# Kernel tuning notes

Hardware: AMD Instinct MI355X
Metric: run time of the kernel (lower is better)

## Reference

```python
import jax, jax.numpy as jnp
import numpy as np

INPUT_SIZE = 512   # num_embeddings == RNN input feature dim
SEQ = INPUT_SIZE // 4   # 128, embedding dim == RNN seq_len
HID = 12
OUT = 3
B = 2048


def setup_inputs() -> dict:
    key = jax.random.key(0)
    ks = jax.random.split(key, 12)
    s = 0.1
    x = jax.random.randint(ks[0], (B, INPUT_SIZE), 0, INPUT_SIZE)
    emb = jax.random.normal(ks[1], (INPUT_SIZE, SEQ), dtype=jnp.float32) * s
    w_ih_f = jax.random.normal(ks[2], (HID, INPUT_SIZE), dtype=jnp.float32) * s
    w_hh_f = jax.random.normal(ks[3], (HID, HID), dtype=jnp.float32) * s
    b_ih_f = jax.random.normal(ks[4], (HID,), dtype=jnp.float32) * s
    b_hh_f = jax.random.normal(ks[5], (HID,), dtype=jnp.float32) * s
    w_ih_r = jax.random.normal(ks[6], (HID, INPUT_SIZE), dtype=jnp.float32) * s
    w_hh_r = jax.random.normal(ks[7], (HID, HID), dtype=jnp.float32) * s
    b_ih_r = jax.random.normal(ks[8], (HID,), dtype=jnp.float32) * s
    b_hh_r = jax.random.normal(ks[9], (HID,), dtype=jnp.float32) * s
    fc_w = jax.random.normal(ks[10], (OUT, 2 * HID), dtype=jnp.float32) * s
    fc_b = jax.random.normal(ks[11], (OUT,), dtype=jnp.float32) * s
    return {"x": x, "emb": emb,
            "w_ih_f": w_ih_f, "w_hh_f": w_hh_f, "b_ih_f": b_ih_f, "b_hh_f": b_hh_f,
            "w_ih_r": w_ih_r, "w_hh_r": w_hh_r, "b_ih_r": b_ih_r, "b_hh_r": b_hh_r,
            "fc_w": fc_w, "fc_b": fc_b}


def reference(x, emb, w_ih_f, w_hh_f, b_ih_f, b_hh_f,
              w_ih_r, w_hh_r, b_ih_r, b_hh_r, fc_w, fc_b):
    # embedding lookup: (B, INPUT_SIZE) -> (B, INPUT_SIZE, SEQ)
    e = emb[x]
    # view(-1, input_size, seq) is a no-op on this contiguous shape; swapaxes(1,2)
    xs = jnp.swapaxes(e, 1, 2)  # (B, SEQ, INPUT_SIZE): seq_len=SEQ, feat=INPUT_SIZE

    # forward-direction tanh RNN: precompute input projections, scan the recurrence
    pre = jnp.einsum('bsi,hi->sbh', xs, w_ih_f) + b_ih_f  # (SEQ, B, HID)

    def step(h, p):
        h = jnp.tanh(p + h @ w_hh_f.T + b_hh_f)
        return h, None

    h0 = jnp.zeros((xs.shape[0], HID), dtype=xs.dtype)
    h_fwd, _ = jax.lax.scan(step, h0, pre)  # final forward hidden (B, HID)

    # reverse-direction output at the LAST timestep = one step from zero hidden
    # on x_{T-1} (only out[:, -1, :] is consumed by the module)
    h_bwd = jnp.tanh(xs[:, -1, :] @ w_ih_r.T + b_ih_r + b_hh_r)  # (B, HID)

    out_last = jnp.concatenate([h_fwd, h_bwd], axis=-1)  # (B, 2*HID)
    return out_last @ fc_w.T + fc_b  # (B, OUT)
```

## Files before the change

kernel.cpp:

```cpp
#include <hip/hip_runtime.h>
#include <hip/hip_bf16.h>

#define B_N     2048
#define IN_N    512
#define SEQ_N   128
#define HID_N   12
#define HP_N    16
#define OUT_N   3

typedef __attribute__((ext_vector_type(8))) short short8;
typedef __attribute__((ext_vector_type(4))) float f32x4;
typedef unsigned int uint;
typedef unsigned short ushort;

__device__ __forceinline__ float fast_tanh(float x) {
    float e = __builtin_amdgcn_exp2f(x * 2.8853900817779268f);
    return 1.0f - 2.0f * __builtin_amdgcn_rcpf(e + 1.0f);
}

__device__ __forceinline__ ushort f2bf(float f) {
    uint u = __float_as_uint(f);
    u += 0x7fffu + ((u >> 16) & 1u);
    return (ushort)(u >> 16);
}

__device__ __forceinline__ float bf2f(ushort s) {
    return __uint_as_float(((uint)s) << 16);
}

__global__ __launch_bounds__(256) void k_prep(
    const float* __restrict__ emb, const float* __restrict__ w_ih_f,
    const float* __restrict__ w_ih_r,
    ushort* __restrict__ embB, ushort* __restrict__ wP)
{
    int tid = blockIdx.x * 256 + threadIdx.x;
    float4 e = ((const float4*)emb)[tid];
    uint2 o;
    o.x = (uint)f2bf(e.x) | ((uint)f2bf(e.y) << 16);
    o.y = (uint)f2bf(e.z) | ((uint)f2bf(e.w) << 16);
    ((uint2*)embB)[tid] = o;

    int j   = tid & 7;
    int l   = (tid >> 3) & 63;
    int src = (tid >> 9) & 1;
    int cks = tid >> 10;
    int h   = l & 15;
    int i   = (cks >> 2) * 128 + (cks & 3) * 32 + (l >> 4) * 8 + j;
    const float* wsrc = src ? w_ih_r : w_ih_f;
    wP[(((size_t)cks * 2 + src) * 64 + l) * 8 + j] =
        (h < HID_N) ? f2bf(wsrc[h * IN_N + i]) : (ushort)0;
}

__global__ __launch_bounds__(256, 4) void k_pre(
    const int* __restrict__ x, const ushort* __restrict__ embB,
    const ushort* __restrict__ wP,
    const float* __restrict__ b_ih_r, const float* __restrict__ b_hh_r,
    ushort* __restrict__ preB, float* __restrict__ rev)
{
    __shared__ int xb[IN_N];
    __shared__ __align__(16) ushort As[128 * 128];

    const int t = threadIdx.x;
    const int b = blockIdx.x;

    ((int2*)xb)[t] = ((const int2*)(x + b * IN_N))[t];
    __syncthreads();

    const int l      = t & 63;
    const int w      = t >> 6;
    const int lane16 = l & 15;
    const int quad   = l >> 4;
    const int il     = w * 32 + quad * 8;
    const int wg     = w * 4 + quad;
    const int l7     = lane16 & 7;

    f32x4 acc[2] = {{0.f,0.f,0.f,0.f},{0.f,0.f,0.f,0.f}};
    f32x4 accR   = {0.f,0.f,0.f,0.f};

    uint R[8][4];

    #pragma unroll
    for (int j = 0; j < 8; ++j) {
        const uint4 v = *(const uint4*)(embB + (size_t)xb[il + j] * SEQ_N + lane16 * 8);
        R[j][0] = v.x; R[j][1] = v.y; R[j][2] = v.z; R[j][3] = v.w;
    }

    for (int c = 0; c < 4; ++c) {
        short8 bfr[4], bfrR[4];
        #pragma unroll
        for (int ks = 0; ks < 4; ++ks) {
            const ushort* wp = wP + ((size_t)(c * 4 + ks) * 128 + l) * 8;
            bfr[ks]  = *(const short8*)(wp);
            bfrR[ks] = *(const short8*)(wp + 512);
        }

        if (c) __syncthreads();

        #pragma unroll
        for (int p = 0; p < 8; ++p) {
            const uint sel = (p & 1) ? 0x07060302u : 0x05040100u;
            const int pv = p >> 1;
            uint u0 = __builtin_amdgcn_perm(R[1][pv], R[0][pv], sel);
            uint u1 = __builtin_amdgcn_perm(R[3][pv], R[2][pv], sel);
            uint u2 = __builtin_amdgcn_perm(R[5][pv], R[4][pv], sel);
            uint u3 = __builtin_amdgcn_perm(R[7][pv], R[6][pv], sel);
            const int s    = lane16 * 8 + p;
            const int slot = wg ^ p ^ l7;
            *(uint4*)&As[(size_t)s * 128 + (size_t)slot * 8] =
                make_uint4(u0, u1, u2, u3);
        }

        if (c < 3) {
            const int ibase = (c + 1) * 128 + il;
            #pragma unroll
            for (int j = 0; j < 8; ++j) {
                const uint4 v = *(const uint4*)(embB + (size_t)xb[ibase + j] * SEQ_N + lane16 * 8);
                R[j][0] = v.x; R[j][1] = v.y; R[j][2] = v.z; R[j][3] = v.w;
            }
        }
        __syncthreads();

        #pragma unroll
        for (int tt = 0; tt < 2; ++tt) {
            const int row = (w * 2 + tt) * 16 + lane16;
            const int fr  = (row & 7) ^ ((row >> 3) & 7);
            #pragma unroll
            for (int ks = 0; ks < 4; ++ks) {
                const int slot = (ks * 4 + quad) ^ fr;
                short8 af = *(const short8*)&As[(size_t)row * 128 + (size_t)slot * 8];
                acc[tt] = __builtin_amdgcn_mfma_f32_16x16x32_bf16(af, bfr[ks], acc[tt], 0, 0, 0);
                if (tt == 1)
                    accR = __builtin_amdgcn_mfma_f32_16x16x32_bf16(af, bfrR[ks], accR, 0, 0, 0);
            }
        }
    }

    if (lane16 < HID_N) {
        #pragma unroll
        for (int tt = 0; tt < 2; ++tt) {
            #pragma unroll
            for (int r = 0; r < 4; ++r) {
                int s = (w * 2 + tt) * 16 + quad * 4 + r;
                preB[((size_t)b * SEQ_N + s) * HP_N + lane16] = f2bf(acc[tt][r]);
            }
        }
        if (w == 3 && quad == 3)
            rev[b * HP_N + lane16] =
                fast_tanh(accR[3] + b_ih_r[lane16] + b_hh_r[lane16]);
    }
}

__global__ __launch_bounds__(256) void k_rnn(
    const ushort* __restrict__ preB, const float* __restrict__ rev,
    const float* __restrict__ w_hh_f,
    const float* __restrict__ b_ih_f, const float* __restrict__ b_hh_f,
    const float* __restrict__ fc_w, const float* __restrict__ fc_b,
    float* __restrict__ out)
{
    __shared__ float ho[16][40];

    const int tid = threadIdx.x;
    const int l   = tid & 63;
    const int j   = l & 15;
    const int jj  = (j < 12) ? j : 0;
    const int gid = tid >> 4;
    const int b   = blockIdx.x * 16 + gid;
    const int baseaddr = (l & 48) << 2;

    const float4* wr = (const float4*)(w_hh_f + jj * 12);
    float4 w0 = wr[0], w1 = wr[1], w2 = wr[2];
    float W[12] = {w0.x, w0.y, w0.z, w0.w, w1.x, w1.y, w1.z, w1.w,
                   w2.x, w2.y, w2.z, w2.w};
    const float bias = b_ih_f[jj] + b_hh_f[jj];

    const ushort* pb = preB + (size_t)b * SEQ_N * HP_N + j;
    ushort pq[8];
    #pragma unroll
    for (int k = 0; k < 8; ++k) pq[k] = pb[k * HP_N];

    float h = 0.f;
    for (int s8 = 0; s8 < 16; ++s8) {
        #pragma unroll
        for (int k = 0; k < 8; ++k) {
            int s = s8 * 8 + k;
            float p = bf2f(pq[k]) + bias;
            pq[k] = pb[((s + 8) & 127) * HP_N];
            int hb = __float_as_int(h);
            float hk[12];
            #pragma unroll
            for (int kk = 0; kk < 12; ++kk)
                hk[kk] = __int_as_float(__builtin_amdgcn_ds_bpermute(baseaddr + 4 * kk, hb));
            float c0 = p, c1 = 0.f, c2 = 0.f;
            #pragma unroll
            for (int u = 0; u < 4; ++u) {
                c0 = __builtin_fmaf(W[u],     hk[u],     c0);
                c1 = __builtin_fmaf(W[4 + u], hk[4 + u], c1);
                c2 = __builtin_fmaf(W[8 + u], hk[8 + u], c2);
            }
            h = fast_tanh(c0 + c1 + c2);
        }
    }

    ho[gid][j]      = h;
    ho[gid][20 + j] = rev[b * HP_N + j];
    if (j < OUT_N) {
        const float* fw = fc_w + j * 24;
        float o = fc_b[j];
        #pragma unroll
        for (int k = 0; k < 12; ++k)
            o += fw[k] * ho[gid][k] + fw[12 + k] * ho[gid][20 + k];
        out[b * OUT_N + j] = o;
    }
}

extern "C" void kernel_launch(void* const* d_in, const int* in_sizes, int n_in,
                              void* d_out, int out_size, void* d_ws, size_t ws_size,
                              hipStream_t stream) {
    const int*   x      = (const int*)  d_in[0];
    const float* emb    = (const float*)d_in[1];
    const float* w_ih_f = (const float*)d_in[2];
    const float* w_hh_f = (const float*)d_in[3];
    const float* b_ih_f = (const float*)d_in[4];
    const float* b_hh_f = (const float*)d_in[5];
    const float* w_ih_r = (const float*)d_in[6];
    const float* b_ih_r = (const float*)d_in[8];
    const float* b_hh_r = (const float*)d_in[9];
    const float* fc_w   = (const float*)d_in[10];
    const float* fc_b   = (const float*)d_in[11];
    float* out = (float*)d_out;

    ushort* preB = (ushort*)d_ws;
    float*  rev  = (float*)((char*)d_ws + 8388608);
    ushort* embB = (ushort*)((char*)d_ws + 8519680);
    ushort* wP   = (ushort*)((char*)d_ws + 8650752);

    k_prep<<<64,   256, 0, stream>>>(emb, w_ih_f, w_ih_r, embB, wP);
    k_pre <<<B_N,  256, 0, stream>>>(x, embB, wP, b_ih_r, b_hh_r, preB, rev);
    k_rnn <<<B_N/16,256,0, stream>>>(preB, rev, w_hh_f, b_ih_f, b_hh_f, fc_w, fc_b, out);
}
```

Measured before the change: 127.1 us.

## Process four batches per k_pre block with LDS-staged weights and software-pipelined gathers

k_pre now handles four batch rows per block, staging the packed bf16 input-projection weights once into LDS and reusing them across all 16 chunk iterations. Gather indices are prefetched two chunks ahead straight from global memory, replacing the shared index buffer, and embedding row loads overlap the MFMA work of the previous chunk, with explicit barriers around the As tile. This amortizes weight loads and block launch overhead. In exchange LDS use doubles, occupancy is capped at 2 blocks per CU, and the grid shrinks to 512 blocks.

```diff
diff --git a/kernel.cpp b/kernel.cpp
--- a/kernel.cpp
+++ b/kernel.cpp
@@ -51,21 +51,16 @@
         (h < HID_N) ? f2bf(wsrc[h * IN_N + i]) : (ushort)0;
 }
 
-__global__ __launch_bounds__(256, 4) void k_pre(
+__global__ __launch_bounds__(256, 2) void k_pre(
     const int* __restrict__ x, const ushort* __restrict__ embB,
     const ushort* __restrict__ wP,
     const float* __restrict__ b_ih_r, const float* __restrict__ b_hh_r,
     ushort* __restrict__ preB, float* __restrict__ rev)
 {
-    __shared__ int xb[IN_N];
     __shared__ __align__(16) ushort As[128 * 128];
-
-    const int t = threadIdx.x;
-    const int b = blockIdx.x;
-
-    ((int2*)xb)[t] = ((const int2*)(x + b * IN_N))[t];
-    __syncthreads();
-
+    __shared__ __align__(16) ushort wPs[16384];
+
+    const int t      = threadIdx.x;
     const int l      = t & 63;
     const int w      = t >> 6;
     const int lane16 = l & 15;
@@ -73,52 +68,78 @@
     const int il     = w * 32 + quad * 8;
     const int wg     = w * 4 + quad;
     const int l7     = lane16 & 7;
-
-    f32x4 acc[2] = {{0.f,0.f,0.f,0.f},{0.f,0.f,0.f,0.f}};
-    f32x4 accR   = {0.f,0.f,0.f,0.f};
-
+    const int so     = lane16 * 8;
+    const int b0     = blockIdx.x * 4;
+
+    {
+        const uint4* s4 = (const uint4*)wP;
+        uint4*       d4 = (uint4*)wPs;
+        #pragma unroll
+        for (int i = 0; i < 8; ++i) d4[t + i * 256] = s4[t + i * 256];
+    }
+
+    f32x4 acc0 = {0.f,0.f,0.f,0.f};
+    f32x4 acc1 = {0.f,0.f,0.f,0.f};
+    f32x4 accR = {0.f,0.f,0.f,0.f};
     uint R[8][4];
 
-    #pragma unroll
-    for (int j = 0; j < 8; ++j) {
-        const uint4 v = *(const uint4*)(embB + (size_t)xb[il + j] * SEQ_N + lane16 * 8);
-        R[j][0] = v.x; R[j][1] = v.y; R[j][2] = v.z; R[j][3] = v.w;
-    }
-
-    for (int c = 0; c < 4; ++c) {
-        short8 bfr[4], bfrR[4];
-        #pragma unroll
-        for (int ks = 0; ks < 4; ++ks) {
-            const ushort* wp = wP + ((size_t)(c * 4 + ks) * 128 + l) * 8;
-            bfr[ks]  = *(const short8*)(wp);
-            bfrR[ks] = *(const short8*)(wp + 512);
-        }
-
-        if (c) __syncthreads();
-
-        #pragma unroll
-        for (int p = 0; p < 8; ++p) {
-            const uint sel = (p & 1) ? 0x07060302u : 0x05040100u;
-            const int pv = p >> 1;
+#define LD8(k, ix) { uint4 v = *(const uint4*)(embB + (size_t)(ix) * SEQ_N + so); \
+        R[k][0]=v.x; R[k][1]=v.y; R[k][2]=v.z; R[k][3]=v.w; }
+
+    int4 nA, nB;
+    {
+        const int* xq = x + (size_t)b0 * IN_N + il;
+        nA = *(const int4*)xq;
+        nB = *(const int4*)(xq + 4);
+    }
+    LD8(0, nA.x) LD8(1, nA.y) LD8(2, nA.z) LD8(3, nA.w)
+    LD8(4, nB.x) LD8(5, nB.y) LD8(6, nB.z) LD8(7, nB.w)
+    {
+        const int* xq = x + (size_t)b0 * IN_N + 128 + il;
+        nA = *(const int4*)xq;
+        nB = *(const int4*)(xq + 4);
+    }
+
+    for (int p = 0; p < 16; ++p) {
+        const int c = p & 3;
+
+        #pragma unroll
+        for (int pp = 0; pp < 8; ++pp) {
+            const uint sel = (pp & 1) ? 0x07060302u : 0x05040100u;
+            const int pv = pp >> 1;
             uint u0 = __builtin_amdgcn_perm(R[1][pv], R[0][pv], sel);
             uint u1 = __builtin_amdgcn_perm(R[3][pv], R[2][pv], sel);
             uint u2 = __builtin_amdgcn_perm(R[5][pv], R[4][pv], sel);
             uint u3 = __builtin_amdgcn_perm(R[7][pv], R[6][pv], sel);
-            const int s    = lane16 * 8 + p;
-            const int slot = wg ^ p ^ l7;
+            const int s    = lane16 * 8 + pp;
+            const int slot = wg ^ pp ^ l7;
             *(uint4*)&As[(size_t)s * 128 + (size_t)slot * 8] =
                 make_uint4(u0, u1, u2, u3);
         }
 
-        if (c < 3) {
-            const int ibase = (c + 1) * 128 + il;
-            #pragma unroll
-            for (int j = 0; j < 8; ++j) {
-                const uint4 v = *(const uint4*)(embB + (size_t)xb[ibase + j] * SEQ_N + lane16 * 8);
-                R[j][0] = v.x; R[j][1] = v.y; R[j][2] = v.z; R[j][3] = v.w;
-            }
-        }
-        __syncthreads();
+        if (p < 15) {
+            LD8(0, nA.x) LD8(1, nA.y) LD8(2, nA.z) LD8(3, nA.w)
+            LD8(4, nB.x) LD8(5, nB.y) LD8(6, nB.z) LD8(7, nB.w)
+            if (p < 14) {
+                const int pn = p + 2;
+                const int* xq = x + (size_t)(b0 + (pn >> 2)) * IN_N
+                                  + (pn & 3) * 128 + il;
+                nA = *(const int4*)xq;
+                nB = *(const int4*)(xq + 4);
+            }
+        }
+
+        asm volatile("s_waitcnt lgkmcnt(0)" ::: "memory");
+        __builtin_amdgcn_s_barrier();
+        __builtin_amdgcn_sched_barrier(0);
+
+        short8 bfr[4], bfrR[4];
+        #pragma unroll
+        for (int ks = 0; ks < 4; ++ks) {
+            const ushort* wp = wPs + (size_t)((c * 4 + ks) * 128 + l) * 8;
+            bfr[ks]  = *(const short8*)wp;
+            bfrR[ks] = *(const short8*)(wp + 512);
+        }
 
         #pragma unroll
         for (int tt = 0; tt < 2; ++tt) {
@@ -128,26 +149,39 @@
             for (int ks = 0; ks < 4; ++ks) {
                 const int slot = (ks * 4 + quad) ^ fr;
                 short8 af = *(const short8*)&As[(size_t)row * 128 + (size_t)slot * 8];
-                acc[tt] = __builtin_amdgcn_mfma_f32_16x16x32_bf16(af, bfr[ks], acc[tt], 0, 0, 0);
-                if (tt == 1)
+                if (tt == 0) {
+                    acc0 = __builtin_amdgcn_mfma_f32_16x16x32_bf16(af, bfr[ks], acc0, 0, 0, 0);
+                } else {
+                    acc1 = __builtin_amdgcn_mfma_f32_16x16x32_bf16(af, bfr[ks], acc1, 0, 0, 0);
                     accR = __builtin_amdgcn_mfma_f32_16x16x32_bf16(af, bfrR[ks], accR, 0, 0, 0);
-            }
-        }
-    }
-
-    if (lane16 < HID_N) {
-        #pragma unroll
-        for (int tt = 0; tt < 2; ++tt) {
-            #pragma unroll
-            for (int r = 0; r < 4; ++r) {
-                int s = (w * 2 + tt) * 16 + quad * 4 + r;
-                preB[((size_t)b * SEQ_N + s) * HP_N + lane16] = f2bf(acc[tt][r]);
-            }
-        }
-        if (w == 3 && quad == 3)
-            rev[b * HP_N + lane16] =
-                fast_tanh(accR[3] + b_ih_r[lane16] + b_hh_r[lane16]);
-    }
+                }
+            }
+        }
+
+        if (c == 3) {
+            const int bcur = b0 + (p >> 2);
+            if (lane16 < HID_N) {
+                #pragma unroll
+                for (int r = 0; r < 4; ++r) {
+                    const int s0v = (w * 2 + 0) * 16 + quad * 4 + r;
+                    preB[((size_t)bcur * SEQ_N + s0v) * HP_N + lane16] = f2bf(acc0[r]);
+                    const int s1v = (w * 2 + 1) * 16 + quad * 4 + r;
+                    preB[((size_t)bcur * SEQ_N + s1v) * HP_N + lane16] = f2bf(acc1[r]);
+                }
+                if (w == 3 && quad == 3)
+                    rev[bcur * HP_N + lane16] =
+                        fast_tanh(accR[3] + b_ih_r[lane16] + b_hh_r[lane16]);
+            }
+            acc0 = (f32x4){0.f,0.f,0.f,0.f};
+            acc1 = (f32x4){0.f,0.f,0.f,0.f};
+            accR = (f32x4){0.f,0.f,0.f,0.f};
+        }
+
+        asm volatile("" ::: "memory");
+        __builtin_amdgcn_s_barrier();
+        __builtin_amdgcn_sched_barrier(0);
+    }
+#undef LD8
 }
 
 __global__ __launch_bounds__(256) void k_rnn(
@@ -234,7 +268,7 @@
     ushort* embB = (ushort*)((char*)d_ws + 8519680);
     ushort* wP   = (ushort*)((char*)d_ws + 8650752);
 
-    k_prep<<<64,   256, 0, stream>>>(emb, w_ih_f, w_ih_r, embB, wP);
-    k_pre <<<B_N,  256, 0, stream>>>(x, embB, wP, b_ih_r, b_hh_r, preB, rev);
-    k_rnn <<<B_N/16,256,0, stream>>>(preB, rev, w_hh_f, b_ih_f, b_hh_f, fc_w, fc_b, out);
-}
+    k_prep<<<64,    256, 0, stream>>>(emb, w_ih_f, w_ih_r, embB, wP);
+    k_pre <<<B_N/4, 256, 0, stream>>>(x, embB, wP, b_ih_r, b_hh_r, preB, rev);
+    k_rnn <<<B_N/16,256, 0, stream>>>(preB, rev, w_hh_f, b_ih_f, b_hh_f, fc_w, fc_b, out);
+}
```

Result: faster. 117.6 us (-7.4%).
